# Optimization experiments

Hardware: AMD Instinct MI355X
Metric: run time of the kernel (lower is better)

## Reference

```python
import jax, jax.numpy as jnp
import numpy as np

DIM = 2048
NUM_HEADS = 16
HEAD_DIM = DIM // NUM_HEADS  # 128
HIDDEN = HEAD_DIM * NUM_HEADS  # 2048


def setup_inputs() -> dict:
    key = jax.random.key(0)
    k1, k2, k3 = jax.random.split(key, 3)
    x = jax.random.normal(k1, (2, 4096, DIM), dtype=jnp.float32)
    # match torch init: gates.weight ~ N(0, dim**-0.5), output.weight ~ N(0, hidden**-0.5)
    Wg = jax.random.normal(k2, (NUM_HEADS + 3 * HIDDEN, DIM), dtype=jnp.float32) * DIM ** -0.5
    bg = jnp.zeros((NUM_HEADS + 3 * HIDDEN,), dtype=jnp.float32)
    Wo = jax.random.normal(k3, (DIM, HIDDEN), dtype=jnp.float32) * HIDDEN ** -0.5
    bo = jnp.zeros((DIM,), dtype=jnp.float32)
    return {"x": x, "Wg": Wg, "bg": bg, "Wo": Wo, "bo": bo}


def _combine(a, b):
    # linear recurrence c_t = f_t * c_{t-1} + u_t as an associative op
    fa, ua = a
    fb, ub = b
    return fa * fb, fb * ua + ub


def reference(x, Wg, bg, Wo, bo):
    # x: [B, T, dim]
    g = jnp.einsum('btd,gd->btg', x, Wg) + bg  # [B, T, H + 3*hidden]
    f = jax.nn.sigmoid(g[..., :NUM_HEADS])  # [B, T, H]
    i = jax.nn.sigmoid(g[..., NUM_HEADS:NUM_HEADS + HIDDEN])
    t = jnp.tanh(g[..., NUM_HEADS + HIDDEN:NUM_HEADS + 2 * HIDDEN])
    o = g[..., NUM_HEADS + 2 * HIDDEN:]
    f = jnp.repeat(f, HEAD_DIM, axis=-1)  # tied forget gate per head -> [B, T, hidden]
    update = i * t
    # scan over time axis (axis=1)
    _, c = jax.lax.associative_scan(_combine, (f, update), axis=1)
    h = o * jnp.tanh(c)
    return jnp.einsum('bth,dh->btd', h, Wo) + bo
```

## Files before the change

### kernel.cpp

```cpp
#include <hip/hip_runtime.h>
#include <hip/hip_bf16.h>

#define DIM 2048
#define NHEADS 16
#define HEAD_DIM 128
#define HIDDEN 2048
#define SEQ 4096
#define BATCH 2
#define BT (BATCH * SEQ)
#define NSEG 64
#define SEGLEN (SEQ / NSEG)
#define N_GATE (3 * HIDDEN)

typedef __bf16 bf16_t;
typedef __bf16 bf16x8 __attribute__((ext_vector_type(8)));
typedef __bf16 bf16x4_t __attribute__((ext_vector_type(4)));
typedef __bf16 bf16x2_t __attribute__((ext_vector_type(2)));
typedef float f32x4 __attribute__((ext_vector_type(4)));

__device__ __forceinline__ void gload_lds16(const void* g, void* l) {
  __builtin_amdgcn_global_load_lds(
      (const __attribute__((address_space(1))) void*)g,
      (__attribute__((address_space(3))) void*)l, 16, 0, 0);
}

#define MEMFENCE asm volatile("" ::: "memory")
#define BAR do { MEMFENCE; __builtin_amdgcn_s_barrier(); MEMFENCE; } while (0)
#define VMCNT(n) asm volatile("s_waitcnt vmcnt(" #n ")" ::: "memory")

__global__ void cvt_f32_bf16(const float* __restrict__ src, bf16_t* __restrict__ dst, int n4) {
  int i = blockIdx.x * blockDim.x + threadIdx.x;
  if (i >= n4) return;
  float4 v = reinterpret_cast<const float4*>(src)[i];
  bf16x4_t o;
  o[0] = (bf16_t)v.x; o[1] = (bf16_t)v.y; o[2] = (bf16_t)v.z; o[3] = (bf16_t)v.w;
  reinterpret_cast<bf16x4_t*>(dst)[i] = o;
}

__global__ void fgate_cvt(const float* __restrict__ x, const float* __restrict__ Wg,
                          const float* __restrict__ bg, float* __restrict__ fout,
                          bf16_t* __restrict__ xb) {
  int idx = blockIdx.x * 256 + threadIdx.x;
  int bt = idx >> 4, h = idx & 15;
  const float* xr = x + (size_t)bt * DIM;
  const float* wr = Wg + (size_t)h * DIM;
  float acc = 0.f;
  for (int k = 0; k < DIM; k += 4) {
    float4 xv = *reinterpret_cast<const float4*>(xr + k);
    float4 wv = *reinterpret_cast<const float4*>(wr + k);
    acc = fmaf(xv.x, wv.x, acc);
    acc = fmaf(xv.y, wv.y, acc);
    acc = fmaf(xv.z, wv.z, acc);
    acc = fmaf(xv.w, wv.w, acc);
  }
  acc += bg[h];
  fout[idx] = 1.f / (1.f + expf(-acc));
  const float* xs = xr + h * HEAD_DIM;
  bf16_t* xd = xb + (size_t)bt * DIM + h * HEAD_DIM;
#pragma unroll
  for (int k = 0; k < HEAD_DIM; k += 8) {
    float4 a = *reinterpret_cast<const float4*>(xs + k);
    float4 b = *reinterpret_cast<const float4*>(xs + k + 4);
    bf16x8 o;
    o[0] = (bf16_t)a.x; o[1] = (bf16_t)a.y; o[2] = (bf16_t)a.z; o[3] = (bf16_t)a.w;
    o[4] = (bf16_t)b.x; o[5] = (bf16_t)b.y; o[6] = (bf16_t)b.z; o[7] = (bf16_t)b.w;
    *reinterpret_cast<bf16x8*>(xd + k) = o;
  }
}


__device__ __forceinline__ void stageA(const bf16_t* __restrict__ G, int brow, int kc,
                                       bf16_t* Aslot, int q, int wid, int lane) {
  const int rr = q * 64 + wid * 8;
  const int grow = brow + (wid >> 2) * 128 + q * 32 + (wid & 3) * 8 + (lane >> 3);
  const int gcol = kc + (((lane & 7) ^ (lane >> 3)) << 3);
  gload_lds16(G + (size_t)grow * 2048 + gcol, Aslot + (size_t)rr * 64);
}

__device__ __forceinline__ void stageB(const bf16_t* __restrict__ G, int bcol, int kc,
                                       bf16_t* Bslot, int j, int wid, int lane) {
  const int rr = (j >> 1) * 128 + (j & 1) * 64 + wid * 8;
  const int grow = bcol + rr + (lane >> 3);
  const int gcol = kc + (((lane & 7) ^ (lane >> 3)) << 3);
  gload_lds16(G + (size_t)grow * 2048 + gcol, Bslot + (size_t)rr * 64);
}

#define FRAG8(ptr, row, fo) (*reinterpret_cast<const bf16x8*>(&(ptr)[(size_t)(row) * 64 + (fo)]))

template <int MODE>
__global__ __launch_bounds__(512, 1)
void gemm256(const bf16_t* __restrict__ A, const bf16_t* __restrict__ B,
             const float* __restrict__ bias,
             bf16_t* __restrict__ Oi, bf16_t* __restrict__ Ot, bf16_t* __restrict__ Oo,
             float* __restrict__ Of, int tiles_n) {
  __shared__ __align__(16) bf16_t As[2][256 * 64];
  __shared__ __align__(16) bf16_t Bs[2][256 * 64];
  constexpr int KT = 32;

  const int tid = threadIdx.x;
  const int wid = tid >> 6, lane = tid & 63;
  const int nwg = gridDim.x, bid = blockIdx.x;
  const int swz = (bid & 7) * (nwg >> 3) + (bid >> 3);
  const int tm = swz / tiles_n, tn = swz - tm * tiles_n;
  const int brow = tm * 256, bcol = tn * 256;
  const int wm = wid >> 2, wn = wid & 3;
  const int rl = lane & 15, qw = lane >> 4;
  const int fo0 = ((qw ^ (rl & 7)) << 3);
  const int fo1 = fo0 ^ 32;
  const int brr = (wn >> 1) * 128 + (wn & 1) * 64;

  f32x4 acc[8][4] = {};

#pragma unroll
  for (int j = 0; j < 4; ++j) stageB(B, bcol, 0, &Bs[0][0], j, wid, lane);
#pragma unroll
  for (int qq = 0; qq < 4; ++qq) stageA(A, brow, 0, &As[0][0], qq, wid, lane);
#pragma unroll
  for (int qq = 0; qq < 3; ++qq) stageA(A, brow, 64, &As[1][0], qq, wid, lane);
  VMCNT(3);
  BAR;

  for (int t = 0; t < KT; ++t) {
    const int s = t & 1, ns = s ^ 1;
    const int kc1 = (t + 1) * 64, kc2 = (t + 2) * 64;
    const bool st1 = (t + 1) < KT, st2 = (t + 2) < KT;
    const bf16_t* Ar = &As[s][0];
    const bf16_t* Br = &Bs[s][0];
    bf16x8 bfr[2][4], af[2][2];

#define MFMA16(p)                                                                         \
  __builtin_amdgcn_s_setprio(1);                                                          \
  _Pragma("unroll")                                                                       \
  for (int mi = 0; mi < 2; ++mi)                                                          \
    _Pragma("unroll")                                                                     \
    for (int ni = 0; ni < 4; ++ni)                                                        \
      acc[(p)*2 + mi][ni] =                                                               \
          __builtin_amdgcn_mfma_f32_16x16x32_bf16(af[0][mi], bfr[0][ni], acc[(p)*2 + mi][ni], 0, 0, 0); \
  _Pragma("unroll")                                                                       \
  for (int mi = 0; mi < 2; ++mi)                                                          \
    _Pragma("unroll")                                                                     \
    for (int ni = 0; ni < 4; ++ni)                                                        \
      acc[(p)*2 + mi][ni] =                                                               \
          __builtin_amdgcn_mfma_f32_16x16x32_bf16(af[1][mi], bfr[1][ni], acc[(p)*2 + mi][ni], 0, 0, 0); \
  __builtin_amdgcn_s_setprio(0)

#pragma unroll
    for (int ni = 0; ni < 4; ++ni) {
      bfr[0][ni] = FRAG8(Br, brr + ni * 16 + rl, fo0);
      bfr[1][ni] = FRAG8(Br, brr + ni * 16 + rl, fo1);
    }
#pragma unroll
    for (int mi = 0; mi < 2; ++mi) {
      af[0][mi] = FRAG8(Ar, 0 * 64 + wm * 32 + mi * 16 + rl, fo0);
      af[1][mi] = FRAG8(Ar, 0 * 64 + wm * 32 + mi * 16 + rl, fo1);
    }
    if (st1) { stageB(B, bcol, kc1, &Bs[ns][0], 0, wid, lane);
               stageB(B, bcol, kc1, &Bs[ns][0], 1, wid, lane); }
    BAR;
    MFMA16(0);

#pragma unroll
    for (int mi = 0; mi < 2; ++mi) {
      af[0][mi] = FRAG8(Ar, 1 * 64 + wm * 32 + mi * 16 + rl, fo0);
      af[1][mi] = FRAG8(Ar, 1 * 64 + wm * 32 + mi * 16 + rl, fo1);
    }
    if (st1) { stageB(B, bcol, kc1, &Bs[ns][0], 2, wid, lane);
               stageB(B, bcol, kc1, &Bs[ns][0], 3, wid, lane); }
    if (t < KT - 1) { VMCNT(4); } else { VMCNT(0); }
    BAR;
    MFMA16(1);

#pragma unroll
    for (int mi = 0; mi < 2; ++mi) {
      af[0][mi] = FRAG8(Ar, 2 * 64 + wm * 32 + mi * 16 + rl, fo0);
      af[1][mi] = FRAG8(Ar, 2 * 64 + wm * 32 + mi * 16 + rl, fo1);
    }
    if (st2) { stageA(A, brow, kc2, &As[s][0], 0, wid, lane);
               stageA(A, brow, kc2, &As[s][0], 1, wid, lane); }
    BAR;
    MFMA16(2);

#pragma unroll
    for (int mi = 0; mi < 2; ++mi) {
      af[0][mi] = FRAG8(Ar, 3 * 64 + wm * 32 + mi * 16 + rl, fo0);
      af[1][mi] = FRAG8(Ar, 3 * 64 + wm * 32 + mi * 16 + rl, fo1);
    }
    if (st2) stageA(A, brow, kc2, &As[s][0], 2, wid, lane);
    if (st1) stageA(A, brow, kc1, &As[ns][0], 3, wid, lane);
    if (t < KT - 2) { VMCNT(4); }
    else if (t == KT - 2) { VMCNT(1); }
    BAR;
    MFMA16(3);
#undef MFMA16
  }

  const int crow0 = brow + wm * 128;
  const int ccol0 = bcol + wn * 64;
  if (MODE == 0) {
    const int section = bcol >> 11;
    bf16_t* dst = (section == 0) ? Oi : ((section == 1) ? Ot : Oo);
#pragma unroll
    for (int mi = 0; mi < 8; ++mi)
#pragma unroll
      for (int ni = 0; ni < 4; ++ni) {
        int gcol = ccol0 + ni * 16 + (lane & 15);
        int col = gcol & 2047;
        float bv = bias[gcol];
#pragma unroll
        for (int qq = 0; qq < 4; ++qq) {
          int row = crow0 + mi * 16 + (lane >> 4) * 4 + qq;
          float v = acc[mi][ni][qq] + bv;
          float aout;
          if (section == 0)      aout = 1.f / (1.f + __expf(-v));
          else if (section == 1) aout = tanhf(v);
          else                   aout = v;
          dst[(size_t)row * HIDDEN + col] = (bf16_t)aout;
        }
      }
  } else {
#pragma unroll
    for (int mi = 0; mi < 8; ++mi)
#pragma unroll
      for (int ni = 0; ni < 4; ++ni) {
        int col = ccol0 + ni * 16 + (lane & 15);
        float bv = bias[col];
#pragma unroll
        for (int qq = 0; qq < 4; ++qq) {
          int row = crow0 + mi * 16 + (lane >> 4) * 4 + qq;
          Of[(size_t)row * DIM + col] = acc[mi][ni][qq] + bv;
        }
      }
  }
}

__global__ void scan_pass1(const float* __restrict__ fg, const bf16_t* __restrict__ gi,
                           const bf16_t* __restrict__ gt, float* __restrict__ cend,
                           float* __restrict__ pseg) {
  int bx = blockIdx.x;
  int chblk = bx & 3, seg = (bx >> 2) & 63, b = bx >> 8;
  int chp = chblk * 256 + threadIdx.x;
  int ch = chp * 2;
  int head = chp >> 6;
  float c0 = 0.f, c1 = 0.f, P = 1.f;
  size_t t0 = (size_t)b * SEQ + (size_t)seg * SEGLEN;
  for (int tt = 0; tt < SEGLEN; ++tt) {
    size_t bt = t0 + tt;
    float f = fg[bt * NHEADS + head];
    bf16x2_t iv = *reinterpret_cast<const bf16x2_t*>(&gi[bt * HIDDEN + ch]);
    bf16x2_t tv = *reinterpret_cast<const bf16x2_t*>(&gt[bt * HIDDEN + ch]);
    c0 = fmaf(f, c0, (float)iv[0] * (float)tv[0]);
    c1 = fmaf(f, c1, (float)iv[1] * (float)tv[1]);
    P *= f;
  }
  size_t o = ((size_t)b * NSEG + seg) * HIDDEN + ch;
  *reinterpret_cast<float2*>(&cend[o]) = make_float2(c0, c1);
  *reinterpret_cast<float2*>(&pseg[o]) = make_float2(P, P);
}

__global__ void scan_pass2(const float* __restrict__ cend, const float* __restrict__ pseg,
                           float* __restrict__ cin) {
  int idx = blockIdx.x * 256 + threadIdx.x;
  int b = idx >> 11, ch = idx & 2047;
  float C = 0.f;
  for (int s = 0; s < NSEG; ++s) {
    size_t o = ((size_t)b * NSEG + s) * HIDDEN + ch;
    cin[o] = C;
    C = cend[o] + pseg[o] * C;
  }
}

__global__ void scan_pass3(const float* __restrict__ fg, const bf16_t* __restrict__ gi,
                           const bf16_t* __restrict__ gt, const bf16_t* __restrict__ go,
                           const float* __restrict__ cin, bf16_t* __restrict__ h) {
  int bx = blockIdx.x;
  int chblk = bx & 3, seg = (bx >> 2) & 63, b = bx >> 8;
  int chp = chblk * 256 + threadIdx.x;
  int ch = chp * 2;
  int head = chp >> 6;
  float2 cv = *reinterpret_cast<const float2*>(&cin[((size_t)b * NSEG + seg) * HIDDEN + ch]);
  float c0 = cv.x, c1 = cv.y;
  size_t t0 = (size_t)b * SEQ + (size_t)seg * SEGLEN;
  for (int tt = 0; tt < SEGLEN; ++tt) {
    size_t bt = t0 + tt;
    float f = fg[bt * NHEADS + head];
    bf16x2_t iv = *reinterpret_cast<const bf16x2_t*>(&gi[bt * HIDDEN + ch]);
    bf16x2_t tv = *reinterpret_cast<const bf16x2_t*>(&gt[bt * HIDDEN + ch]);
    bf16x2_t ov = *reinterpret_cast<const bf16x2_t*>(&go[bt * HIDDEN + ch]);
    c0 = fmaf(f, c0, (float)iv[0] * (float)tv[0]);
    c1 = fmaf(f, c1, (float)iv[1] * (float)tv[1]);
    bf16x2_t hv;
    hv[0] = (bf16_t)((float)ov[0] * tanhf(c0));
    hv[1] = (bf16_t)((float)ov[1] * tanhf(c1));
    *reinterpret_cast<bf16x2_t*>(&h[bt * HIDDEN + ch]) = hv;
  }
}

extern "C" void kernel_launch(void* const* d_in, const int* in_sizes, int n_in,
                              void* d_out, int out_size, void* d_ws, size_t ws_size,
                              hipStream_t stream) {
  const float* x  = (const float*)d_in[0];
  const float* Wg = (const float*)d_in[1];
  const float* bg = (const float*)d_in[2];
  const float* Wo = (const float*)d_in[3];
  const float* bo = (const float*)d_in[4];
  float* out = (float*)d_out;

  char* ws = (char*)d_ws;
  size_t off = 0;
  auto alloc = [&](size_t bytes) -> void* {
    void* p = ws + off;
    off += (bytes + 255) & ~(size_t)255;
    return p;
  };
  bf16_t* xb   = (bf16_t*)alloc((size_t)BT * DIM * 2);
  bf16_t* wgb  = (bf16_t*)alloc((size_t)N_GATE * DIM * 2);
  bf16_t* wob  = (bf16_t*)alloc((size_t)DIM * HIDDEN * 2);
  float*  fg   = (float*)alloc((size_t)BT * NHEADS * 4);
  bf16_t* gi   = (bf16_t*)alloc((size_t)BT * HIDDEN * 2);
  bf16_t* gt   = (bf16_t*)alloc((size_t)BT * HIDDEN * 2);
  bf16_t* go   = (bf16_t*)alloc((size_t)BT * HIDDEN * 2);
  bf16_t* hbuf = (bf16_t*)alloc((size_t)BT * HIDDEN * 2);
  float*  cend = (float*)alloc((size_t)BATCH * NSEG * HIDDEN * 4);
  float*  pseg = (float*)alloc((size_t)BATCH * NSEG * HIDDEN * 4);
  float*  cin  = (float*)alloc((size_t)BATCH * NSEG * HIDDEN * 4);
  (void)ws_size; (void)in_sizes; (void)n_in; (void)out_size;

  {
    int n4 = N_GATE * DIM / 4;
    cvt_f32_bf16<<<(n4 + 255) / 256, 256, 0, stream>>>(Wg + (size_t)NHEADS * DIM, wgb, n4);
  }
  {
    int n4 = DIM * HIDDEN / 4;
    cvt_f32_bf16<<<(n4 + 255) / 256, 256, 0, stream>>>(Wo, wob, n4);
  }

  fgate_cvt<<<(BT * NHEADS) / 256, 256, 0, stream>>>(x, Wg, bg, fg, xb);

  gemm256<0><<<768, 512, 0, stream>>>(xb, wgb, bg + NHEADS, gi, gt, go, nullptr, 24);

  scan_pass1<<<BATCH * NSEG * (HIDDEN / 512), 256, 0, stream>>>(fg, gi, gt, cend, pseg);
  scan_pass2<<<BATCH * HIDDEN / 256, 256, 0, stream>>>(cend, pseg, cin);
  scan_pass3<<<BATCH * NSEG * (HIDDEN / 512), 256, 0, stream>>>(fg, gi, gt, go, cin, hbuf);

  gemm256<1><<<256, 512, 0, stream>>>(hbuf, wob, bo, nullptr, nullptr, nullptr, out, 8);
}
```

Baseline: 509.2 us.

## Replace 256x256 GEMM tile with 128x128 tile, two blocks per CU

Both GEMMs move from a 256x256 output tile with 8 waves and a finely interleaved multi-barrier pipeline to a 128x128 tile with 4 waves and simple double buffering, with one barrier per K-step. The goal is more workgroups, up to two resident per CU, and simpler scheduling, so latency is hidden by occupancy instead of a hand-tuned staging pipeline. In exchange, operand reuse per tile is halved, so global and L2 traffic roughly doubles. Each K-step also waits for all of its loads (vmcnt 0), which may expose memory latency.

```diff
diff --git a/kernel.cpp b/kernel.cpp
--- a/kernel.cpp
+++ b/kernel.cpp
@@ -69,146 +69,102 @@
 }
 
 
-__device__ __forceinline__ void stageA(const bf16_t* __restrict__ G, int brow, int kc,
-                                       bf16_t* Aslot, int q, int wid, int lane) {
-  const int rr = q * 64 + wid * 8;
-  const int grow = brow + (wid >> 2) * 128 + q * 32 + (wid & 3) * 8 + (lane >> 3);
-  const int gcol = kc + (((lane & 7) ^ (lane >> 3)) << 3);
-  gload_lds16(G + (size_t)grow * 2048 + gcol, Aslot + (size_t)rr * 64);
-}
-
-__device__ __forceinline__ void stageB(const bf16_t* __restrict__ G, int bcol, int kc,
-                                       bf16_t* Bslot, int j, int wid, int lane) {
-  const int rr = (j >> 1) * 128 + (j & 1) * 64 + wid * 8;
-  const int grow = bcol + rr + (lane >> 3);
-  const int gcol = kc + (((lane & 7) ^ (lane >> 3)) << 3);
-  gload_lds16(G + (size_t)grow * 2048 + gcol, Bslot + (size_t)rr * 64);
+__device__ __forceinline__ void stage_u(const bf16_t* __restrict__ G, int grow0, int kc,
+                                        bf16_t* region, int u, int tid) {
+  const int row = u * 32 + (tid >> 3);
+  const int c = (tid & 7) ^ ((tid >> 3) & 7);
+  gload_lds16(G + (size_t)(grow0 + row) * 2048 + kc + c * 8,
+              region + (size_t)(u * 32 + (tid >> 6) * 8) * 64);
 }
 
 #define FRAG8(ptr, row, fo) (*reinterpret_cast<const bf16x8*>(&(ptr)[(size_t)(row) * 64 + (fo)]))
 
 template <int MODE>
-__global__ __launch_bounds__(512, 1)
-void gemm256(const bf16_t* __restrict__ A, const bf16_t* __restrict__ B,
+__global__ __launch_bounds__(256, 2)
+void gemm128(const bf16_t* __restrict__ A, const bf16_t* __restrict__ B,
              const float* __restrict__ bias,
              bf16_t* __restrict__ Oi, bf16_t* __restrict__ Ot, bf16_t* __restrict__ Oo,
              float* __restrict__ Of, int tiles_n) {
-  __shared__ __align__(16) bf16_t As[2][256 * 64];
-  __shared__ __align__(16) bf16_t Bs[2][256 * 64];
+  __shared__ __align__(16) bf16_t As[2][128 * 64];
+  __shared__ __align__(16) bf16_t Bs[2][128 * 64];
   constexpr int KT = 32;
 
   const int tid = threadIdx.x;
-  const int wid = tid >> 6, lane = tid & 63;
+  const int lane = tid & 63;
+  const int wid = tid >> 6;
   const int nwg = gridDim.x, bid = blockIdx.x;
   const int swz = (bid & 7) * (nwg >> 3) + (bid >> 3);
   const int tm = swz / tiles_n, tn = swz - tm * tiles_n;
-  const int brow = tm * 256, bcol = tn * 256;
-  const int wm = wid >> 2, wn = wid & 3;
+  const int brow = tm * 128, bcol = tn * 128;
+  const int wm = wid >> 1, wn = wid & 1;
   const int rl = lane & 15, qw = lane >> 4;
   const int fo0 = ((qw ^ (rl & 7)) << 3);
   const int fo1 = fo0 ^ 32;
-  const int brr = (wn >> 1) * 128 + (wn & 1) * 64;
-
-  f32x4 acc[8][4] = {};
-
-#pragma unroll
-  for (int j = 0; j < 4; ++j) stageB(B, bcol, 0, &Bs[0][0], j, wid, lane);
-#pragma unroll
-  for (int qq = 0; qq < 4; ++qq) stageA(A, brow, 0, &As[0][0], qq, wid, lane);
-#pragma unroll
-  for (int qq = 0; qq < 3; ++qq) stageA(A, brow, 64, &As[1][0], qq, wid, lane);
-  VMCNT(3);
+
+  f32x4 acc[4][4] = {};
+
+#pragma unroll
+  for (int u = 0; u < 4; ++u) stage_u(B, bcol, 0, &Bs[0][0], u, tid);
+#pragma unroll
+  for (int u = 0; u < 4; ++u) stage_u(A, brow, 0, &As[0][0], u, tid);
+  VMCNT(0);
   BAR;
 
   for (int t = 0; t < KT; ++t) {
     const int s = t & 1, ns = s ^ 1;
-    const int kc1 = (t + 1) * 64, kc2 = (t + 2) * 64;
-    const bool st1 = (t + 1) < KT, st2 = (t + 2) < KT;
+    const int kc1 = (t + 1) * 64;
+    const bool st1 = (t + 1) < KT;
     const bf16_t* Ar = &As[s][0];
     const bf16_t* Br = &Bs[s][0];
-    bf16x8 bfr[2][4], af[2][2];
-
-#define MFMA16(p)                                                                         \
-  __builtin_amdgcn_s_setprio(1);                                                          \
-  _Pragma("unroll")                                                                       \
-  for (int mi = 0; mi < 2; ++mi)                                                          \
-    _Pragma("unroll")                                                                     \
-    for (int ni = 0; ni < 4; ++ni)                                                        \
-      acc[(p)*2 + mi][ni] =                                                               \
-          __builtin_amdgcn_mfma_f32_16x16x32_bf16(af[0][mi], bfr[0][ni], acc[(p)*2 + mi][ni], 0, 0, 0); \
-  _Pragma("unroll")                                                                       \
-  for (int mi = 0; mi < 2; ++mi)                                                          \
-    _Pragma("unroll")                                                                     \
-    for (int ni = 0; ni < 4; ++ni)                                                        \
-      acc[(p)*2 + mi][ni] =                                                               \
-          __builtin_amdgcn_mfma_f32_16x16x32_bf16(af[1][mi], bfr[1][ni], acc[(p)*2 + mi][ni], 0, 0, 0); \
-  __builtin_amdgcn_s_setprio(0)
-
+    bf16x8 afr[2][4], bfr[2][4];
+
+#pragma unroll
+    for (int mi = 0; mi < 4; ++mi) {
+      afr[0][mi] = FRAG8(Ar, wm * 64 + mi * 16 + rl, fo0);
+      afr[1][mi] = FRAG8(Ar, wm * 64 + mi * 16 + rl, fo1);
+    }
 #pragma unroll
     for (int ni = 0; ni < 4; ++ni) {
-      bfr[0][ni] = FRAG8(Br, brr + ni * 16 + rl, fo0);
-      bfr[1][ni] = FRAG8(Br, brr + ni * 16 + rl, fo1);
+      bfr[0][ni] = FRAG8(Br, wn * 64 + ni * 16 + rl, fo0);
+      bfr[1][ni] = FRAG8(Br, wn * 64 + ni * 16 + rl, fo1);
     }
-#pragma unroll
-    for (int mi = 0; mi < 2; ++mi) {
-      af[0][mi] = FRAG8(Ar, 0 * 64 + wm * 32 + mi * 16 + rl, fo0);
-      af[1][mi] = FRAG8(Ar, 0 * 64 + wm * 32 + mi * 16 + rl, fo1);
+    if (st1) {
+#pragma unroll
+      for (int u = 0; u < 4; ++u) stage_u(B, bcol, kc1, &Bs[ns][0], u, tid);
+#pragma unroll
+      for (int u = 0; u < 4; ++u) stage_u(A, brow, kc1, &As[ns][0], u, tid);
     }
-    if (st1) { stageB(B, bcol, kc1, &Bs[ns][0], 0, wid, lane);
-               stageB(B, bcol, kc1, &Bs[ns][0], 1, wid, lane); }
+    __builtin_amdgcn_s_setprio(1);
+#pragma unroll
+    for (int mi = 0; mi < 4; ++mi)
+#pragma unroll
+      for (int ni = 0; ni < 4; ++ni)
+        acc[mi][ni] = __builtin_amdgcn_mfma_f32_16x16x32_bf16(afr[0][mi], bfr[0][ni], acc[mi][ni], 0, 0, 0);
+#pragma unroll
+    for (int mi = 0; mi < 4; ++mi)
+#pragma unroll
+      for (int ni = 0; ni < 4; ++ni)
+        acc[mi][ni] = __builtin_amdgcn_mfma_f32_16x16x32_bf16(afr[1][mi], bfr[1][ni], acc[mi][ni], 0, 0, 0);
+    __builtin_amdgcn_s_setprio(0);
+    if (st1) { VMCNT(0); }
     BAR;
-    MFMA16(0);
-
-#pragma unroll
-    for (int mi = 0; mi < 2; ++mi) {
-      af[0][mi] = FRAG8(Ar, 1 * 64 + wm * 32 + mi * 16 + rl, fo0);
-      af[1][mi] = FRAG8(Ar, 1 * 64 + wm * 32 + mi * 16 + rl, fo1);
-    }
-    if (st1) { stageB(B, bcol, kc1, &Bs[ns][0], 2, wid, lane);
-               stageB(B, bcol, kc1, &Bs[ns][0], 3, wid, lane); }
-    if (t < KT - 1) { VMCNT(4); } else { VMCNT(0); }
-    BAR;
-    MFMA16(1);
-
-#pragma unroll
-    for (int mi = 0; mi < 2; ++mi) {
-      af[0][mi] = FRAG8(Ar, 2 * 64 + wm * 32 + mi * 16 + rl, fo0);
-      af[1][mi] = FRAG8(Ar, 2 * 64 + wm * 32 + mi * 16 + rl, fo1);
-    }
-    if (st2) { stageA(A, brow, kc2, &As[s][0], 0, wid, lane);
-               stageA(A, brow, kc2, &As[s][0], 1, wid, lane); }
-    BAR;
-    MFMA16(2);
-
-#pragma unroll
-    for (int mi = 0; mi < 2; ++mi) {
-      af[0][mi] = FRAG8(Ar, 3 * 64 + wm * 32 + mi * 16 + rl, fo0);
-      af[1][mi] = FRAG8(Ar, 3 * 64 + wm * 32 + mi * 16 + rl, fo1);
-    }
-    if (st2) stageA(A, brow, kc2, &As[s][0], 2, wid, lane);
-    if (st1) stageA(A, brow, kc1, &As[ns][0], 3, wid, lane);
-    if (t < KT - 2) { VMCNT(4); }
-    else if (t == KT - 2) { VMCNT(1); }
-    BAR;
-    MFMA16(3);
-#undef MFMA16
-  }
-
-  const int crow0 = brow + wm * 128;
+  }
+
+  const int crow0 = brow + wm * 64;
   const int ccol0 = bcol + wn * 64;
   if (MODE == 0) {
     const int section = bcol >> 11;
     bf16_t* dst = (section == 0) ? Oi : ((section == 1) ? Ot : Oo);
 #pragma unroll
-    for (int mi = 0; mi < 8; ++mi)
+    for (int mi = 0; mi < 4; ++mi)
 #pragma unroll
       for (int ni = 0; ni < 4; ++ni) {
-        int gcol = ccol0 + ni * 16 + (lane & 15);
+        int gcol = ccol0 + ni * 16 + rl;
         int col = gcol & 2047;
         float bv = bias[gcol];
 #pragma unroll
         for (int qq = 0; qq < 4; ++qq) {
-          int row = crow0 + mi * 16 + (lane >> 4) * 4 + qq;
+          int row = crow0 + mi * 16 + qw * 4 + qq;
           float v = acc[mi][ni][qq] + bv;
           float aout;
           if (section == 0)      aout = 1.f / (1.f + __expf(-v));
@@ -219,14 +175,14 @@
       }
   } else {
 #pragma unroll
-    for (int mi = 0; mi < 8; ++mi)
+    for (int mi = 0; mi < 4; ++mi)
 #pragma unroll
       for (int ni = 0; ni < 4; ++ni) {
-        int col = ccol0 + ni * 16 + (lane & 15);
+        int col = ccol0 + ni * 16 + rl;
         float bv = bias[col];
 #pragma unroll
         for (int qq = 0; qq < 4; ++qq) {
-          int row = crow0 + mi * 16 + (lane >> 4) * 4 + qq;
+          int row = crow0 + mi * 16 + qw * 4 + qq;
           Of[(size_t)row * DIM + col] = acc[mi][ni][qq] + bv;
         }
       }
@@ -336,11 +292,11 @@
 
   fgate_cvt<<<(BT * NHEADS) / 256, 256, 0, stream>>>(x, Wg, bg, fg, xb);
 
-  gemm256<0><<<768, 512, 0, stream>>>(xb, wgb, bg + NHEADS, gi, gt, go, nullptr, 24);
+  gemm128<0><<<3072, 256, 0, stream>>>(xb, wgb, bg + NHEADS, gi, gt, go, nullptr, 48);
 
   scan_pass1<<<BATCH * NSEG * (HIDDEN / 512), 256, 0, stream>>>(fg, gi, gt, cend, pseg);
   scan_pass2<<<BATCH * HIDDEN / 256, 256, 0, stream>>>(cend, pseg, cin);
   scan_pass3<<<BATCH * NSEG * (HIDDEN / 512), 256, 0, stream>>>(fg, gi, gt, go, cin, hbuf);
 
-  gemm256<1><<<256, 512, 0, stream>>>(hbuf, wob, bo, nullptr, nullptr, nullptr, out, 8);
-}
+  gemm128<1><<<1024, 256, 0, stream>>>(hbuf, wob, bo, nullptr, nullptr, nullptr, out, 16);
+}
```

After: 568.9 us. +11.7%, slower.

## Interleave i/t gate weight rows so GEMM epilogue writes fused update i*t

Applied to the files above, without the earlier changes.

The gate weight conversion now interleaves input-gate and tanh-gate rows, so adjacent GEMM output columns hold matching i and t values. The epilogue combines them with a lane shuffle and writes a single bf16 update buffer instead of separate i and t buffers. This removes one full activation tensor write from the GEMM and one read from each scan pass. The two weight conversion launches are merged into one kernel. Only half the lanes store, with stride-1 columns, which may reduce store coalescing in the epilogue.

```diff
diff --git a/kernel.cpp b/kernel.cpp
--- a/kernel.cpp
+++ b/kernel.cpp
@@ -28,13 +28,29 @@
 #define BAR do { MEMFENCE; __builtin_amdgcn_s_barrier(); MEMFENCE; } while (0)
 #define VMCNT(n) asm volatile("s_waitcnt vmcnt(" #n ")" ::: "memory")
 
-__global__ void cvt_f32_bf16(const float* __restrict__ src, bf16_t* __restrict__ dst, int n4) {
-  int i = blockIdx.x * blockDim.x + threadIdx.x;
-  if (i >= n4) return;
-  float4 v = reinterpret_cast<const float4*>(src)[i];
+__global__ void cvt_weights(const float* __restrict__ Wg, bf16_t* __restrict__ wgb,
+                            const float* __restrict__ Wo, bf16_t* __restrict__ wob) {
+  int i = blockIdx.x * 256 + threadIdx.x;
+  const int n4g = N_GATE * DIM / 4;
+  const int n4o = DIM * HIDDEN / 4;
+  const float* s;
+  bf16_t* d;
+  if (i < n4g) {
+    int r = i >> 9;
+    int j = i & 511;
+    int src = (r < 4096) ? (NHEADS + (r & 1) * HIDDEN + (r >> 1))
+                         : (NHEADS + 2 * HIDDEN + (r - 4096));
+    s = Wg + (size_t)src * DIM + j * 4;
+    d = wgb + (size_t)r * DIM + j * 4;
+  } else if (i < n4g + n4o) {
+    int j = i - n4g;
+    s = Wo + (size_t)j * 4;
+    d = wob + (size_t)j * 4;
+  } else return;
+  float4 v = *reinterpret_cast<const float4*>(s);
   bf16x4_t o;
   o[0] = (bf16_t)v.x; o[1] = (bf16_t)v.y; o[2] = (bf16_t)v.z; o[3] = (bf16_t)v.w;
-  reinterpret_cast<bf16x4_t*>(dst)[i] = o;
+  *reinterpret_cast<bf16x4_t*>(d) = o;
 }
 
 __global__ void fgate_cvt(const float* __restrict__ x, const float* __restrict__ Wg,
@@ -91,7 +107,7 @@
 __global__ __launch_bounds__(512, 1)
 void gemm256(const bf16_t* __restrict__ A, const bf16_t* __restrict__ B,
              const float* __restrict__ bias,
-             bf16_t* __restrict__ Oi, bf16_t* __restrict__ Ot, bf16_t* __restrict__ Oo,
+             bf16_t* __restrict__ Ou, bf16_t* __restrict__ Oo,
              float* __restrict__ Of, int tiles_n) {
   __shared__ __align__(16) bf16_t As[2][256 * 64];
   __shared__ __align__(16) bf16_t Bs[2][256 * 64];
@@ -197,24 +213,29 @@
   const int crow0 = brow + wm * 128;
   const int ccol0 = bcol + wn * 64;
   if (MODE == 0) {
-    const int section = bcol >> 11;
-    bf16_t* dst = (section == 0) ? Oi : ((section == 1) ? Ot : Oo);
+    const bool osec = (bcol >= 4096);
 #pragma unroll
     for (int mi = 0; mi < 8; ++mi)
 #pragma unroll
       for (int ni = 0; ni < 4; ++ni) {
         int gcol = ccol0 + ni * 16 + (lane & 15);
-        int col = gcol & 2047;
-        float bv = bias[gcol];
+        int bidx = osec ? (2 * HIDDEN + (gcol - 4096))
+                        : ((gcol & 1) * HIDDEN + (gcol >> 1));
+        float bv = bias[bidx];
 #pragma unroll
         for (int qq = 0; qq < 4; ++qq) {
           int row = crow0 + mi * 16 + (lane >> 4) * 4 + qq;
           float v = acc[mi][ni][qq] + bv;
-          float aout;
-          if (section == 0)      aout = 1.f / (1.f + __expf(-v));
-          else if (section == 1) aout = tanhf(v);
-          else                   aout = v;
-          dst[(size_t)row * HIDDEN + col] = (bf16_t)aout;
+          if (osec) {
+            Oo[(size_t)row * HIDDEN + (gcol - 4096)] = (bf16_t)v;
+          } else {
+            float a = (gcol & 1) ? tanhf(v) : (1.f / (1.f + __expf(-v)));
+            float partner = __shfl_xor(a, 1);
+            if (!(gcol & 1)) {
+              float u = a * partner;
+              Ou[(size_t)row * HIDDEN + (gcol >> 1)] = (bf16_t)u;
+            }
+          }
         }
       }
   } else {
@@ -233,12 +254,11 @@
   }
 }
 
-__global__ void scan_pass1(const float* __restrict__ fg, const bf16_t* __restrict__ gi,
-                           const bf16_t* __restrict__ gt, float* __restrict__ cend,
-                           float* __restrict__ pseg) {
+__global__ void scan_pass1(const float* __restrict__ fg, const bf16_t* __restrict__ u,
+                           float* __restrict__ cend, float* __restrict__ pseg) {
   int bx = blockIdx.x;
-  int chblk = bx & 3, seg = (bx >> 2) & 63, b = bx >> 8;
-  int chp = chblk * 256 + threadIdx.x;
+  int gblk = bx & 3, seg = (bx >> 2) & 63, b = bx >> 8;
+  int chp = gblk * 256 + threadIdx.x;
   int ch = chp * 2;
   int head = chp >> 6;
   float c0 = 0.f, c1 = 0.f, P = 1.f;
@@ -246,10 +266,9 @@
   for (int tt = 0; tt < SEGLEN; ++tt) {
     size_t bt = t0 + tt;
     float f = fg[bt * NHEADS + head];
-    bf16x2_t iv = *reinterpret_cast<const bf16x2_t*>(&gi[bt * HIDDEN + ch]);
-    bf16x2_t tv = *reinterpret_cast<const bf16x2_t*>(&gt[bt * HIDDEN + ch]);
-    c0 = fmaf(f, c0, (float)iv[0] * (float)tv[0]);
-    c1 = fmaf(f, c1, (float)iv[1] * (float)tv[1]);
+    bf16x2_t uv = *reinterpret_cast<const bf16x2_t*>(&u[bt * HIDDEN + ch]);
+    c0 = fmaf(f, c0, (float)uv[0]);
+    c1 = fmaf(f, c1, (float)uv[1]);
     P *= f;
   }
   size_t o = ((size_t)b * NSEG + seg) * HIDDEN + ch;
@@ -269,12 +288,12 @@
   }
 }
 
-__global__ void scan_pass3(const float* __restrict__ fg, const bf16_t* __restrict__ gi,
-                           const bf16_t* __restrict__ gt, const bf16_t* __restrict__ go,
-                           const float* __restrict__ cin, bf16_t* __restrict__ h) {
+__global__ void scan_pass3(const float* __restrict__ fg, const bf16_t* __restrict__ u,
+                           const bf16_t* __restrict__ go, const float* __restrict__ cin,
+                           bf16_t* __restrict__ h) {
   int bx = blockIdx.x;
-  int chblk = bx & 3, seg = (bx >> 2) & 63, b = bx >> 8;
-  int chp = chblk * 256 + threadIdx.x;
+  int gblk = bx & 3, seg = (bx >> 2) & 63, b = bx >> 8;
+  int chp = gblk * 256 + threadIdx.x;
   int ch = chp * 2;
   int head = chp >> 6;
   float2 cv = *reinterpret_cast<const float2*>(&cin[((size_t)b * NSEG + seg) * HIDDEN + ch]);
@@ -283,11 +302,10 @@
   for (int tt = 0; tt < SEGLEN; ++tt) {
     size_t bt = t0 + tt;
     float f = fg[bt * NHEADS + head];
-    bf16x2_t iv = *reinterpret_cast<const bf16x2_t*>(&gi[bt * HIDDEN + ch]);
-    bf16x2_t tv = *reinterpret_cast<const bf16x2_t*>(&gt[bt * HIDDEN + ch]);
+    bf16x2_t uv = *reinterpret_cast<const bf16x2_t*>(&u[bt * HIDDEN + ch]);
     bf16x2_t ov = *reinterpret_cast<const bf16x2_t*>(&go[bt * HIDDEN + ch]);
-    c0 = fmaf(f, c0, (float)iv[0] * (float)tv[0]);
-    c1 = fmaf(f, c1, (float)iv[1] * (float)tv[1]);
+    c0 = fmaf(f, c0, (float)uv[0]);
+    c1 = fmaf(f, c1, (float)uv[1]);
     bf16x2_t hv;
     hv[0] = (bf16_t)((float)ov[0] * tanhf(c0));
     hv[1] = (bf16_t)((float)ov[1] * tanhf(c1));
@@ -316,8 +334,7 @@
   bf16_t* wgb  = (bf16_t*)alloc((size_t)N_GATE * DIM * 2);
   bf16_t* wob  = (bf16_t*)alloc((size_t)DIM * HIDDEN * 2);
   float*  fg   = (float*)alloc((size_t)BT * NHEADS * 4);
-  bf16_t* gi   = (bf16_t*)alloc((size_t)BT * HIDDEN * 2);
-  bf16_t* gt   = (bf16_t*)alloc((size_t)BT * HIDDEN * 2);
+  bf16_t* ubuf = (bf16_t*)alloc((size_t)BT * HIDDEN * 2);
   bf16_t* go   = (bf16_t*)alloc((size_t)BT * HIDDEN * 2);
   bf16_t* hbuf = (bf16_t*)alloc((size_t)BT * HIDDEN * 2);
   float*  cend = (float*)alloc((size_t)BATCH * NSEG * HIDDEN * 4);
@@ -326,21 +343,17 @@
   (void)ws_size; (void)in_sizes; (void)n_in; (void)out_size;
 
   {
-    int n4 = N_GATE * DIM / 4;
-    cvt_f32_bf16<<<(n4 + 255) / 256, 256, 0, stream>>>(Wg + (size_t)NHEADS * DIM, wgb, n4);
-  }
-  {
-    int n4 = DIM * HIDDEN / 4;
-    cvt_f32_bf16<<<(n4 + 255) / 256, 256, 0, stream>>>(Wo, wob, n4);
+    int nthread = N_GATE * DIM / 4 + DIM * HIDDEN / 4;
+    cvt_weights<<<(nthread + 255) / 256, 256, 0, stream>>>(Wg, wgb, Wo, wob);
   }
 
   fgate_cvt<<<(BT * NHEADS) / 256, 256, 0, stream>>>(x, Wg, bg, fg, xb);
 
-  gemm256<0><<<768, 512, 0, stream>>>(xb, wgb, bg + NHEADS, gi, gt, go, nullptr, 24);
-
-  scan_pass1<<<BATCH * NSEG * (HIDDEN / 512), 256, 0, stream>>>(fg, gi, gt, cend, pseg);
+  gemm256<0><<<768, 512, 0, stream>>>(xb, wgb, bg + NHEADS, ubuf, go, nullptr, 24);
+
+  scan_pass1<<<BATCH * NSEG * 4, 256, 0, stream>>>(fg, ubuf, cend, pseg);
   scan_pass2<<<BATCH * HIDDEN / 256, 256, 0, stream>>>(cend, pseg, cin);
-  scan_pass3<<<BATCH * NSEG * (HIDDEN / 512), 256, 0, stream>>>(fg, gi, gt, go, cin, hbuf);
-
-  gemm256<1><<<256, 512, 0, stream>>>(hbuf, wob, bo, nullptr, nullptr, nullptr, out, 8);
-}
+  scan_pass3<<<BATCH * NSEG * 4, 256, 0, stream>>>(fg, ubuf, go, cin, hbuf);
+
+  gemm256<1><<<256, 512, 0, stream>>>(hbuf, wob, bo, nullptr, nullptr, out, 8);
+}
```

Result: slower. 689.2 us (+35.3%).
